# Optimization experiments

Measured on AMD Instinct MI355X. Metric: run time of the kernel, lower is better.

## Reference

```python
import jax, jax.numpy as jnp
import numpy as np

H, NH, R = 128, 8, 6
NB = 2                  # geometric interaction blocks
BS, L, K = 16, 64, 16   # graphs, blocks/graph, atoms/block
NBLK = BS * L           # 1024 blocks total
N = NBLK * K            # 16384 atoms
E = 262144              # atom-level edges
EB = 512                # block-level edges per graph
CUTOFF = 8.0


def _mha(x, in_w, in_b, out_w, out_b):
    # torch nn.MultiheadAttention (batch_first, eval / no dropout). x: [B,S,H]
    B_, S, _ = x.shape
    qkv = x @ in_w + in_b                     # [B,S,3H]
    q, k, v = jnp.split(qkv, 3, axis=-1)
    dh = H // NH
    q = q.reshape(B_, S, NH, dh)
    k = k.reshape(B_, S, NH, dh)
    v = v.reshape(B_, S, NH, dh)
    scores = jnp.einsum('bind,bjnd->bnij', q, k) / np.sqrt(dh).astype(np.float32)
    attn = jax.nn.softmax(scores, axis=-1)
    o = jnp.einsum('bnij,bjnd->bind', attn, v).reshape(B_, S, H)
    return o @ out_w + out_b


def _forward(A, atom_positions, B_types, coords, edge_index, block_edges,
             emb_atom, emb_pos, emb_block, rbf_freq,
             inter_w1, inter_b1, inter_w2, inter_b2,
             upd_w1, upd_b1, upd_w2, upd_b2,
             edge_w1, edge_b1, edge_w2, edge_b2,
             attn_in_w, attn_in_b, attn_out_w, attn_out_b,
             ln_g, ln_b, fin_w1, fin_b1, fin_w2, fin_b2, fin_w3, fin_b3):
    block_id = jnp.repeat(jnp.arange(NBLK), K)  # uniform K atoms per block
    # atom embedding + position embedding + broadcast block embedding
    x = emb_atom[A] + emb_pos[atom_positions] + emb_block[B_types][block_id]  # [N,H]

    # ---- GeometricAtomProcessor ----
    i, j = edge_index[0], edge_index[1]
    d = jnp.linalg.norm(coords[i] - coords[j], axis=-1)       # [E]
    u = jnp.clip(d / CUTOFF, 1e-3, None)
    # DimeNet envelope, exponent=5 -> p=6: 1/u + a u^5 + b u^6 + c u^7
    env = 1.0 / u - 28.0 * u**5 + 48.0 * u**6 - 21.0 * u**7
    rbf = env[:, None] * jnp.sin(rbf_freq[None, :] * u[:, None])  # [E,R]

    for b in range(NB):
        ef = jnp.concatenate([x[i], x[j], rbf], axis=-1)       # [E,2H+R] gather
        m = jax.nn.silu(ef @ inter_w1[b] + inter_b1[b]) @ inter_w2[b] + inter_b2[b]
        agg = jax.ops.segment_sum(m, i, num_segments=N)        # index_add_ scatter
        ui = jnp.concatenate([x, agg], axis=-1)
        x = jax.nn.silu(ui @ upd_w1[b] + upd_b1[b]) @ upd_w2[b] + upd_b2[b] + x

    # scatter_mean over block_id (uniform blocks -> reshape mean)
    blocks = x.reshape(NBLK, K, H).mean(axis=1).reshape(BS, L, H)

    # ---- per-graph block-edge attention (batched over graphs) ----
    src, dst = block_edges[..., 0], block_edges[..., 1]        # [BS,EB]
    bidx = jnp.arange(BS)[:, None]
    ef = jnp.concatenate([blocks[bidx, src], blocks[bidx, dst]], axis=-1)  # [BS,EB,2H]
    ef = jax.nn.relu(ef @ edge_w1 + edge_b1) @ edge_w2 + edge_b2
    ea = _mha(ef, attn_in_w, attn_in_b, attn_out_w, attn_out_b)            # [BS,EB,H]
    seg = (src + bidx * L).reshape(-1)
    sums = jax.ops.segment_sum(ea.reshape(-1, H), seg, num_segments=NBLK)
    cnt = jax.ops.segment_sum(jnp.ones((BS * EB,), ea.dtype), seg, num_segments=NBLK)
    blocks = blocks + (sums / jnp.maximum(cnt, 1.0)[:, None]).reshape(BS, L, H)

    # ---- block self-attention + mean pool ----
    att = _mha(blocks, attn_in_w, attn_in_b, attn_out_w, attn_out_b)
    g = att.mean(axis=1)                                       # [BS,H]
    mu = g.mean(-1, keepdims=True)
    var = ((g - mu) ** 2).mean(-1, keepdims=True)
    g = (g - mu) / jnp.sqrt(var + 1e-5) * ln_g + ln_b
    h1 = jax.nn.relu(g @ fin_w1 + fin_b1)
    h2 = jax.nn.relu(h1 @ fin_w2 + fin_b2)
    return (h2 @ fin_w3 + fin_b3).squeeze(-1)                  # [BS]


def setup_inputs() -> dict:
    key = jax.random.key(0)
    ks = jax.random.split(key, 40)
    def nrm(k, shape, s=0.05):
        return jax.random.normal(k, shape, jnp.float32) * s
    inp = {}
    inp['A'] = jax.random.randint(ks[0], (N,), 0, 100)
    inp['atom_positions'] = jax.random.randint(ks[1], (N,), 0, 16)
    inp['B_types'] = jax.random.randint(ks[2], (NBLK,), 0, 1000)
    inp['coords'] = jax.random.uniform(ks[3], (N, 3), jnp.float32, 0.0, 20.0)
    inp['edge_index'] = jax.random.randint(ks[4], (2, E), 0, N)
    inp['block_edges'] = jax.random.randint(ks[5], (BS, EB, 2), 0, L)
    inp['emb_atom'] = nrm(ks[6], (100, H), 0.5)
    inp['emb_pos'] = nrm(ks[7], (16, H), 0.5)
    inp['emb_block'] = nrm(ks[8], (1000, H), 0.5)
    inp['rbf_freq'] = (jnp.arange(1, R + 1, dtype=jnp.float32) * np.pi)
    inp['inter_w1'] = nrm(ks[9], (NB, 2 * H + R, H))
    inp['inter_b1'] = jnp.zeros((NB, H), jnp.float32)
    inp['inter_w2'] = nrm(ks[10], (NB, H, H))
    inp['inter_b2'] = jnp.zeros((NB, H), jnp.float32)
    inp['upd_w1'] = nrm(ks[11], (NB, 2 * H, H))
    inp['upd_b1'] = jnp.zeros((NB, H), jnp.float32)
    inp['upd_w2'] = nrm(ks[12], (NB, H, H))
    inp['upd_b2'] = jnp.zeros((NB, H), jnp.float32)
    inp['edge_w1'] = nrm(ks[13], (2 * H, H))
    inp['edge_b1'] = jnp.zeros((H,), jnp.float32)
    inp['edge_w2'] = nrm(ks[14], (H, H))
    inp['edge_b2'] = jnp.zeros((H,), jnp.float32)
    inp['attn_in_w'] = nrm(ks[15], (H, 3 * H))
    inp['attn_in_b'] = jnp.zeros((3 * H,), jnp.float32)
    inp['attn_out_w'] = nrm(ks[16], (H, H))
    inp['attn_out_b'] = jnp.zeros((H,), jnp.float32)
    inp['ln_g'] = jnp.ones((H,), jnp.float32)
    inp['ln_b'] = jnp.zeros((H,), jnp.float32)
    inp['fin_w1'] = nrm(ks[17], (H, H))
    inp['fin_b1'] = jnp.zeros((H,), jnp.float32)
    inp['fin_w2'] = nrm(ks[18], (H, H))
    inp['fin_b2'] = jnp.zeros((H,), jnp.float32)
    inp['fin_w3'] = nrm(ks[19], (H, 1))
    inp['fin_b3'] = jnp.zeros((1,), jnp.float32)
    return inp


def reference(A, atom_positions, B_types, coords, edge_index, block_edges,
              emb_atom, emb_pos, emb_block, rbf_freq,
              inter_w1, inter_b1, inter_w2, inter_b2,
              upd_w1, upd_b1, upd_w2, upd_b2,
              edge_w1, edge_b1, edge_w2, edge_b2,
              attn_in_w, attn_in_b, attn_out_w, attn_out_b,
              ln_g, ln_b, fin_w1, fin_b1, fin_w2, fin_b2, fin_w3, fin_b3):
    return _forward(A, atom_positions, B_types, coords, edge_index, block_edges,
                    emb_atom, emb_pos, emb_block, rbf_freq,
                    inter_w1, inter_b1, inter_w2, inter_b2,
                    upd_w1, upd_b1, upd_w2, upd_b2,
                    edge_w1, edge_b1, edge_w2, edge_b2,
                    attn_in_w, attn_in_b, attn_out_w, attn_out_b,
                    ln_g, ln_b, fin_w1, fin_b1, fin_w2, fin_b2, fin_w3, fin_b3)
```

## Files before the change

kernel.cpp:

```cpp
#include <hip/hip_runtime.h>
#include <math.h>

#define H 128
#define NHD 8
#define DH 16
#define RB 6
#define NBI 2
#define BSG 16
#define LBLK 64
#define KATOM 16
#define NBLKT 1024
#define NA 16384
#define NE 262144
#define EBE 512

__device__ __forceinline__ float atomAddF(float* p, float v) {
#if defined(__gfx90a__) || defined(__gfx940__) || defined(__gfx941__) || defined(__gfx942__) || defined(__gfx950__)
  return unsafeAtomicAdd(p, v);
#else
  return atomicAdd(p, v);
#endif
}

__device__ __forceinline__ float fsilu(float v) {
  return v * __builtin_amdgcn_rcpf(1.0f + __expf(-v));
}

typedef short v4s __attribute__((ext_vector_type(4)));
typedef float f32x4 __attribute__((ext_vector_type(4)));

__device__ __forceinline__ short f2bf(float f) {
  union { float f; unsigned u; } v; v.f = f;
  unsigned r = v.u + 0x7fffu + ((v.u >> 16) & 1u);
  return (short)(r >> 16);
}

#if defined(__has_builtin)
#if __has_builtin(__builtin_amdgcn_mfma_f32_16x16x16bf16_1k)
#define HAVE_MFMA16_1K 1
#endif
#endif

#ifdef HAVE_MFMA16_1K
__device__ __forceinline__ f32x4 mfma16(v4s a, v4s b, f32x4 c) {
  return __builtin_amdgcn_mfma_f32_16x16x16bf16_1k(a, b, c, 0, 0, 0);
}
#else
typedef short v8s __attribute__((ext_vector_type(8)));
__device__ __forceinline__ f32x4 mfma16(v4s a, v4s b, f32x4 c) {
  v8s a8 = {a[0], a[1], a[2], a[3], 0, 0, 0, 0};
  v8s b8 = {b[0], b[1], b[2], b[3], 0, 0, 0, 0};
  return __builtin_amdgcn_mfma_f32_16x16x32_bf16(a8, b8, c, 0, 0, 0);
}
#endif

__global__ __launch_bounds__(256) void k_embed(
    const int* __restrict__ A, const int* __restrict__ apos,
    const int* __restrict__ btypes,
    const float* __restrict__ emb_atom, const float* __restrict__ emb_pos,
    const float* __restrict__ emb_block, float* __restrict__ x)
{
  int idx = blockIdx.x * 256 + threadIdx.x;
  int n = idx >> 7, h = idx & 127;
  x[idx] = emb_atom[A[n] * H + h] + emb_pos[apos[n] * H + h]
         + emb_block[btypes[n >> 4] * H + h];
}

__global__ __launch_bounds__(256) void k_hist(
    const int* __restrict__ ei, int* __restrict__ cnt)
{
  int e = blockIdx.x * 256 + threadIdx.x;
  atomicAdd(&cnt[ei[e]], 1);
}

__global__ __launch_bounds__(1024) void k_scan(
    const int* __restrict__ cnt, int* __restrict__ off,
    int* __restrict__ cur, float* __restrict__ cntf)
{
  __shared__ int ps[1024];
  int t = threadIdx.x;
  int base = t * 16;
  int local[16];
  int s = 0;
  #pragma unroll
  for (int k = 0; k < 16; ++k) { local[k] = s; s += cnt[base + k]; }
  ps[t] = s;
  __syncthreads();
  for (int d = 1; d < 1024; d <<= 1) {
    int v = (t >= d) ? ps[t - d] : 0;
    __syncthreads();
    ps[t] += v;
    __syncthreads();
  }
  int offset = (t == 0) ? 0 : ps[t - 1];
  #pragma unroll
  for (int k = 0; k < 16; ++k) {
    int o = offset + local[k];
    off[base + k] = o;
    cur[base + k] = o;
    cntf[base + k] = (float)cnt[base + k];
  }
  if (t == 1023) off[NA] = offset + s;
}

__global__ __launch_bounds__(256) void k_scatter(
    const int* __restrict__ ei, const int* __restrict__ ej,
    const float* __restrict__ coords, const float* __restrict__ freq,
    int* __restrict__ cur, int* __restrict__ ej_s, float* __restrict__ rbf_s)
{
  int e = blockIdx.x * 256 + threadIdx.x;
  int i = ei[e], j = ej[e];
  int pos = atomicAdd(&cur[i], 1);
  ej_s[pos] = j;
  float dx = coords[i*3+0] - coords[j*3+0];
  float dy = coords[i*3+1] - coords[j*3+1];
  float dz = coords[i*3+2] - coords[j*3+2];
  float d = sqrtf(dx*dx + dy*dy + dz*dz);
  float u = fmaxf(d * 0.125f, 1e-3f);
  float u2 = u*u, u4 = u2*u2, u5 = u4*u, u6 = u5*u, u7 = u6*u;
  float env = 1.0f/u - 28.0f*u5 + 48.0f*u6 - 21.0f*u7;
  #pragma unroll
  for (int r = 0; r < RB; ++r)
    rbf_s[(size_t)pos*RB + r] = env * sinf(freq[r] * u);
}

__global__ __launch_bounds__(256) void k_bedge_csr(
    const int* __restrict__ bedges, int* __restrict__ blist,
    int* __restrict__ boff, float* __restrict__ ind)
{
  __shared__ int hist[64], offs[65], curs[64];
  int b = blockIdx.x, t = threadIdx.x;
  if (t < 64) hist[t] = 0;
  __syncthreads();
  for (int e = t; e < EBE; e += 256) atomicAdd(&hist[bedges[(b*EBE + e)*2]], 1);
  __syncthreads();
  if (t == 0) {
    offs[0] = 0;
    for (int k = 0; k < 64; ++k) offs[k+1] = offs[k] + hist[k];
  }
  __syncthreads();
  if (t < 64) curs[t] = offs[t];
  __syncthreads();
  for (int e = t; e < EBE; e += 256) {
    int src = bedges[(b*EBE + e)*2];
    int pos = atomicAdd(&curs[src], 1);
    blist[b*EBE + pos] = e;
  }
  if (t < 65) boff[b*65 + t] = offs[t];
  if (t < 64) ind[b*64 + t] = (hist[t] > 0) ? 1.0f : 0.0f;
}

__global__ __launch_bounds__(256) void k_edge_csr(
    const float* __restrict__ P, const float* __restrict__ Q,
    const float* __restrict__ rbf_s, const float* __restrict__ W1c,
    const int* __restrict__ ej_s, const int* __restrict__ off,
    float* __restrict__ Hagg)
{
  __shared__ float w[RB * H];
  for (int idx = threadIdx.x; idx < RB * H; idx += 256) w[idx] = W1c[idx];
  __syncthreads();
  int c4 = threadIdx.x & 31;
  int sub = threadIdx.x >> 5;
  int i = blockIdx.x * 8 + sub;
  int e0 = off[i], e1 = off[i + 1];
  float4 pv = *(const float4*)&P[(size_t)i * H + c4 * 4];
  float4 W0 = *(const float4*)&w[0*H + c4*4];
  float4 W1 = *(const float4*)&w[1*H + c4*4];
  float4 W2 = *(const float4*)&w[2*H + c4*4];
  float4 W3 = *(const float4*)&w[3*H + c4*4];
  float4 W4 = *(const float4*)&w[4*H + c4*4];
  float4 W5 = *(const float4*)&w[5*H + c4*4];
  float4 acc = {0, 0, 0, 0};
  for (int e = e0; e < e1; ++e) {
    int j = ej_s[e];
    float4 qv = *(const float4*)&Q[(size_t)j * H + c4 * 4];
    const float* rb = &rbf_s[(size_t)e * RB];
    float r0 = rb[0], r1 = rb[1], r2 = rb[2], r3 = rb[3], r4 = rb[4], r5 = rb[5];
    float4 v;
    v.x = pv.x + qv.x + r0*W0.x + r1*W1.x + r2*W2.x + r3*W3.x + r4*W4.x + r5*W5.x;
    v.y = pv.y + qv.y + r0*W0.y + r1*W1.y + r2*W2.y + r3*W3.y + r4*W4.y + r5*W5.y;
    v.z = pv.z + qv.z + r0*W0.z + r1*W1.z + r2*W2.z + r3*W3.z + r4*W4.z + r5*W5.z;
    v.w = pv.w + qv.w + r0*W0.w + r1*W1.w + r2*W2.w + r3*W3.w + r4*W4.w + r5*W5.w;
    acc.x += fsilu(v.x);
    acc.y += fsilu(v.y);
    acc.z += fsilu(v.z);
    acc.w += fsilu(v.w);
  }
  *(float4*)&Hagg[(size_t)i * H + c4 * 4] = acc;
}

__global__ __launch_bounds__(128) void k_wprep(
    const float* __restrict__ W2base, const float* __restrict__ U1base,
    const float* __restrict__ b2base, float* __restrict__ bvecbase,
    short* __restrict__ wt_u1base)
{
  int y = blockIdx.y;
  const float* W2 = W2base + (size_t)y * H * H;
  const float* U1 = U1base + (size_t)y * 2 * H * H;
  const float* b2 = b2base + y * H;
  float* bvec = bvecbase + y * H;
  short* wt1 = wt_u1base + (size_t)y * 128 * 256;
  int k = blockIdx.x, c = threadIdx.x;
  const float* U1b = U1 + 128 * H;
  wt1[c * 256 + k] = f2bf(U1[k * H + c]);
  float s = 0.0f;
  for (int t = 0; t < H; ++t) s += W2[k * H + t] * U1b[t * H + c];
  wt1[c * 256 + 128 + k] = f2bf(s);
  if (k == 0) {
    float sb = 0.0f;
    for (int t = 0; t < H; ++t) sb += b2[t] * U1b[t * H + c];
    bvec[c] = sb;
  }
}

__global__ __launch_bounds__(256) void k_tcvt(
    const float* __restrict__ inter_w1, const float* __restrict__ upd_w2,
    short* __restrict__ wt_pq, short* __restrict__ wt_u2)
{
  int idx = blockIdx.x * 256 + threadIdx.x;
  {
    int k = idx & 127, col = (idx >> 7) & 127, y = (idx >> 14) & 1, b = idx >> 15;
    wt_pq[idx] = f2bf(inter_w1[((size_t)b*262 + y*128 + k)*128 + col]);
  }
  if (idx < 2*128*128) {
    int k = idx & 127, col = (idx >> 7) & 127, b = idx >> 14;
    wt_u2[idx] = f2bf(upd_w2[((size_t)b*128 + k)*128 + col]);
  }
}

__global__ __launch_bounds__(256) void k_pq_mfma(
    const float* __restrict__ x, const short* __restrict__ WtPQ,
    const float* __restrict__ b1,
    float* __restrict__ P, float* __restrict__ Q)
{
  __shared__ short As[64][136];
  __shared__ short Ws[128][72];
  int tid = threadIdx.x;
  int m0 = blockIdx.x * 64;
  int y = blockIdx.y;
  const short* Wt = WtPQ + (size_t)y * 128 * 128;
  float* C = y ? Q : P;
  for (int idx = tid; idx < 64*32; idx += 256) {
    int r = idx >> 5, c4 = idx & 31;
    float4 v = *(const float4*)&x[(size_t)(m0 + r)*H + c4*4];
    short4 s4 = { f2bf(v.x), f2bf(v.y), f2bf(v.z), f2bf(v.w) };
    *(short4*)&As[r][c4*4] = s4;
  }
  int lane = tid & 63, wv = tid >> 6;
  int c = lane & 15, g = lane >> 4;
  int rowb = wv * 16;
  f32x4 acc[8];
  #pragma unroll
  for (int t = 0; t < 8; ++t) acc[t] = (f32x4){0,0,0,0};
  for (int kc = 0; kc < 2; ++kc) {
    __syncthreads();
    {
      int col = tid >> 1, hh = (tid & 1) * 32;
      const int4* src = (const int4*)&Wt[col*128 + kc*64 + hh];
      int4 a0 = src[0], a1 = src[1], a2 = src[2], a3 = src[3];
      *(int4*)&Ws[col][hh] = a0;      *(int4*)&Ws[col][hh+8] = a1;
      *(int4*)&Ws[col][hh+16] = a2;   *(int4*)&Ws[col][hh+24] = a3;
    }
    __syncthreads();
    #pragma unroll
    for (int ks = 0; ks < 4; ++ks) {
      v4s a = *(const v4s*)&As[rowb + c][kc*64 + ks*16 + g*4];
      #pragma unroll
      for (int ct = 0; ct < 8; ++ct) {
        v4s bf = *(const v4s*)&Ws[ct*16 + c][ks*16 + g*4];
        acc[ct] = mfma16(a, bf, acc[ct]);
      }
    }
  }
  #pragma unroll
  for (int ct = 0; ct < 8; ++ct) {
    int col = ct*16 + c;
    float bb = y ? 0.0f : b1[col];
    #pragma unroll
    for (int r = 0; r < 4; ++r) {
      int row = m0 + rowb + g*4 + r;
      C[(size_t)row*H + col] = acc[ct][r] + bb;
    }
  }
}

__global__ __launch_bounds__(256) void k_upd_mfma(
    const float* __restrict__ x, const float* __restrict__ Hagg,
    const short* __restrict__ Wt1,
    const float* __restrict__ b1, const float* __restrict__ bvec,
    const float* __restrict__ cntf,
    const short* __restrict__ Wt2,
    const float* __restrict__ b2,
    float* __restrict__ xout)
{
  __shared__ short As[64][264];
  __shared__ short Ws[128][72];
  __shared__ short Us[64][136];
  int tid = threadIdx.x;
  int m0 = blockIdx.x * 64;
  for (int idx = tid; idx < 64*64; idx += 256) {
    int r = idx >> 6, c4 = idx & 63;
    const float* src = (c4 < 32) ? &x[(size_t)(m0 + r)*H + c4*4]
                                 : &Hagg[(size_t)(m0 + r)*H + (c4-32)*4];
    float4 v = *(const float4*)src;
    short4 s4 = { f2bf(v.x), f2bf(v.y), f2bf(v.z), f2bf(v.w) };
    *(short4*)&As[r][c4*4] = s4;
  }
  int lane = tid & 63, wv = tid >> 6;
  int c = lane & 15, g = lane >> 4;
  int rowb = wv * 16;
  f32x4 acc[8];
  #pragma unroll
  for (int t = 0; t < 8; ++t) acc[t] = (f32x4){0,0,0,0};
  for (int kc = 0; kc < 4; ++kc) {
    __syncthreads();
    {
      int col = tid >> 1, hh = (tid & 1) * 32;
      const int4* src = (const int4*)&Wt1[col*256 + kc*64 + hh];
      int4 a0 = src[0], a1 = src[1], a2 = src[2], a3 = src[3];
      *(int4*)&Ws[col][hh] = a0;      *(int4*)&Ws[col][hh+8] = a1;
      *(int4*)&Ws[col][hh+16] = a2;   *(int4*)&Ws[col][hh+24] = a3;
    }
    __syncthreads();
    #pragma unroll
    for (int ks = 0; ks < 4; ++ks) {
      v4s a = *(const v4s*)&As[rowb + c][kc*64 + ks*16 + g*4];
      #pragma unroll
      for (int ct = 0; ct < 8; ++ct) {
        v4s bf = *(const v4s*)&Ws[ct*16 + c][ks*16 + g*4];
        acc[ct] = mfma16(a, bf, acc[ct]);
      }
    }
  }
  {
    float cr[4];
    #pragma unroll
    for (int r = 0; r < 4; ++r) cr[r] = cntf[m0 + rowb + g*4 + r];
    #pragma unroll
    for (int ct = 0; ct < 8; ++ct) {
      int col = ct*16 + c;
      float bb = b1[col], bv = bvec[col];
      #pragma unroll
      for (int r = 0; r < 4; ++r) {
        float v = acc[ct][r] + bb + bv * cr[r];
        Us[rowb + g*4 + r][col] = f2bf(fsilu(v));
        acc[ct][r] = 0.0f;
      }
    }
  }
  for (int kc = 0; kc < 2; ++kc) {
    __syncthreads();
    {
      int col = tid >> 1, hh = (tid & 1) * 32;
      const int4* src = (const int4*)&Wt2[col*128 + kc*64 + hh];
      int4 a0 = src[0], a1 = src[1], a2 = src[2], a3 = src[3];
      *(int4*)&Ws[col][hh] = a0;      *(int4*)&Ws[col][hh+8] = a1;
      *(int4*)&Ws[col][hh+16] = a2;   *(int4*)&Ws[col][hh+24] = a3;
    }
    __syncthreads();
    #pragma unroll
    for (int ks = 0; ks < 4; ++ks) {
      v4s a = *(const v4s*)&Us[rowb + c][kc*64 + ks*16 + g*4];
      #pragma unroll
      for (int ct = 0; ct < 8; ++ct) {
        v4s bf = *(const v4s*)&Ws[ct*16 + c][ks*16 + g*4];
        acc[ct] = mfma16(a, bf, acc[ct]);
      }
    }
  }
  #pragma unroll
  for (int ct = 0; ct < 8; ++ct) {
    int col = ct*16 + c;
    float bb = b2[col];
    #pragma unroll
    for (int r = 0; r < 4; ++r) {
      int row = m0 + rowb + g*4 + r;
      xout[(size_t)row*H + col] = acc[ct][r] + bb + x[(size_t)row*H + col];
    }
  }
}

__global__ __launch_bounds__(256) void gemm128(
    const float* __restrict__ A1, const float* __restrict__ A2,
    const float* __restrict__ W, int ldw, int wcol0,
    const float* __restrict__ bias, const float* __restrict__ bias2,
    const float* __restrict__ bias_scale,
    const float* __restrict__ res,
    float* __restrict__ C, int ldc, int ccol0,
    int M, int Ktot, int act, int ymul, int wrowmul, long long cymul)
{
  __shared__ float As[32][256];
  __shared__ float Ws[16][128];
  int tid = threadIdx.x;
  int m0 = blockIdx.x * 32;
  int yoff = blockIdx.y * ymul;
  W += (size_t)blockIdx.y * wrowmul * ldw;
  C += (size_t)blockIdx.y * cymul;
  bool doBias = (ymul != 0) || (blockIdx.y == 0);
  for (int idx = tid; idx < 32*32; idx += 256) {
    int r = idx >> 5, k4 = idx & 31;
    float4 v = *(const float4*)&A1[(size_t)(m0 + r)*H + k4*4];
    *(float4*)&As[r][k4*4] = v;
  }
  if (A2) {
    for (int idx = tid; idx < 32*32; idx += 256) {
      int r = idx >> 5, k4 = idx & 31;
      float4 v = *(const float4*)&A2[(size_t)(m0 + r)*H + k4*4];
      *(float4*)&As[r][128 + k4*4] = v;
    }
  }
  int rr = tid >> 5;
  int cq = tid & 31;
  float acc[4][4] = {};
  for (int kk0 = 0; kk0 < Ktot; kk0 += 16) {
    __syncthreads();
    for (int idx = tid; idx < 16*32; idx += 256) {
      int kr = idx >> 5, c4 = idx & 31;
      float4 v = *(const float4*)&W[(size_t)(kk0 + kr)*ldw + wcol0 + yoff + c4*4];
      *(float4*)&Ws[kr][c4*4] = v;
    }
    __syncthreads();
    #pragma unroll
    for (int k4 = 0; k4 < 4; ++k4) {
      float4 w0 = *(const float4*)&Ws[k4*4+0][cq*4];
      float4 w1 = *(const float4*)&Ws[k4*4+1][cq*4];
      float4 w2 = *(const float4*)&Ws[k4*4+2][cq*4];
      float4 w3 = *(const float4*)&Ws[k4*4+3][cq*4];
      #pragma unroll
      for (int i = 0; i < 4; ++i) {
        float4 a = *(const float4*)&As[rr + 8*i][kk0 + k4*4];
        acc[i][0] += a.x*w0.x + a.y*w1.x + a.z*w2.x + a.w*w3.x;
        acc[i][1] += a.x*w0.y + a.y*w1.y + a.z*w2.y + a.w*w3.y;
        acc[i][2] += a.x*w0.z + a.y*w1.z + a.z*w2.z + a.w*w3.z;
        acc[i][3] += a.x*w0.w + a.y*w1.w + a.z*w2.w + a.w*w3.w;
      }
    }
  }
  #pragma unroll
  for (int i = 0; i < 4; ++i) {
    int m = m0 + rr + 8*i;
    float bs = bias_scale ? bias_scale[m] : 1.0f;
    float4 out;
    float* po = &out.x;
    #pragma unroll
    for (int j = 0; j < 4; ++j) {
      int c = cq*4 + j;
      float v = acc[i][j];
      if (bias && doBias) v += bias[yoff + c];
      if (bias2 && doBias) v += bias2[yoff + c] * bs;
      if (act == 1) v = fsilu(v);
      else if (act == 2) v = fmaxf(v, 0.0f);
      if (res) v += res[(size_t)m*H + c];
      po[j] = v;
    }
    *(float4*)&C[(size_t)m*ldc + ccol0 + yoff + cq*4] = out;
  }
}

__global__ __launch_bounds__(256) void k_eprep(
    const float* __restrict__ Pb, const float* __restrict__ Qb,
    const int* __restrict__ bedges,
    const float* __restrict__ W2e, const float* __restrict__ b2e,
    const float* __restrict__ Win, const float* __restrict__ bin,
    float* __restrict__ qkv)
{
  __shared__ float As[32][128];
  __shared__ float Ws[16][128];
  __shared__ float Us[32][128];
  int tid = threadIdx.x;
  int m0 = blockIdx.x * 32;
  int chunk = blockIdx.y;
  for (int idx = tid; idx < 32*32; idx += 256) {
    int r = idx >> 5, k4 = idx & 31;
    int row = m0 + r;
    int g = row >> 9;
    int src = bedges[row*2], dst = bedges[row*2 + 1];
    float4 pv = *(const float4*)&Pb[(size_t)(g*LBLK + src)*H + k4*4];
    float4 qv = *(const float4*)&Qb[(size_t)(g*LBLK + dst)*H + k4*4];
    float4 v;
    v.x = fmaxf(pv.x + qv.x, 0.0f);
    v.y = fmaxf(pv.y + qv.y, 0.0f);
    v.z = fmaxf(pv.z + qv.z, 0.0f);
    v.w = fmaxf(pv.w + qv.w, 0.0f);
    *(float4*)&As[r][k4*4] = v;
  }
  int rr = tid >> 5;
  int cq = tid & 31;
  float acc[4][4] = {};
  for (int kk0 = 0; kk0 < 128; kk0 += 16) {
    __syncthreads();
    for (int idx = tid; idx < 16*32; idx += 256) {
      int kr = idx >> 5, c4 = idx & 31;
      *(float4*)&Ws[kr][c4*4] = *(const float4*)&W2e[(size_t)(kk0 + kr)*H + c4*4];
    }
    __syncthreads();
    #pragma unroll
    for (int k4 = 0; k4 < 4; ++k4) {
      float4 w0 = *(const float4*)&Ws[k4*4+0][cq*4];
      float4 w1 = *(const float4*)&Ws[k4*4+1][cq*4];
      float4 w2 = *(const float4*)&Ws[k4*4+2][cq*4];
      float4 w3 = *(const float4*)&Ws[k4*4+3][cq*4];
      #pragma unroll
      for (int i = 0; i < 4; ++i) {
        float4 a = *(const float4*)&As[rr + 8*i][kk0 + k4*4];
        acc[i][0] += a.x*w0.x + a.y*w1.x + a.z*w2.x + a.w*w3.x;
        acc[i][1] += a.x*w0.y + a.y*w1.y + a.z*w2.y + a.w*w3.y;
        acc[i][2] += a.x*w0.z + a.y*w1.z + a.z*w2.z + a.w*w3.z;
        acc[i][3] += a.x*w0.w + a.y*w1.w + a.z*w2.w + a.w*w3.w;
      }
    }
  }
  #pragma unroll
  for (int i = 0; i < 4; ++i) {
    float4 u;
    float* pu = &u.x;
    #pragma unroll
    for (int j = 0; j < 4; ++j) pu[j] = acc[i][j] + b2e[cq*4 + j];
    *(float4*)&Us[rr + 8*i][cq*4] = u;
    acc[i][0] = 0.0f; acc[i][1] = 0.0f; acc[i][2] = 0.0f; acc[i][3] = 0.0f;
  }
  for (int kk0 = 0; kk0 < 128; kk0 += 16) {
    __syncthreads();
    for (int idx = tid; idx < 16*32; idx += 256) {
      int kr = idx >> 5, c4 = idx & 31;
      *(float4*)&Ws[kr][c4*4] =
          *(const float4*)&Win[(size_t)(kk0 + kr)*384 + chunk*128 + c4*4];
    }
    __syncthreads();
    #pragma unroll
    for (int k4 = 0; k4 < 4; ++k4) {
      float4 w0 = *(const float4*)&Ws[k4*4+0][cq*4];
      float4 w1 = *(const float4*)&Ws[k4*4+1][cq*4];
      float4 w2 = *(const float4*)&Ws[k4*4+2][cq*4];
      float4 w3 = *(const float4*)&Ws[k4*4+3][cq*4];
      #pragma unroll
      for (int i = 0; i < 4; ++i) {
        float4 a = *(const float4*)&Us[rr + 8*i][kk0 + k4*4];
        acc[i][0] += a.x*w0.x + a.y*w1.x + a.z*w2.x + a.w*w3.x;
        acc[i][1] += a.x*w0.y + a.y*w1.y + a.z*w2.y + a.w*w3.y;
        acc[i][2] += a.x*w0.z + a.y*w1.z + a.z*w2.z + a.w*w3.z;
        acc[i][3] += a.x*w0.w + a.y*w1.w + a.z*w2.w + a.w*w3.w;
      }
    }
  }
  #pragma unroll
  for (int i = 0; i < 4; ++i) {
    int m = m0 + rr + 8*i;
    float4 out;
    float* po = &out.x;
    #pragma unroll
    for (int j = 0; j < 4; ++j)
      po[j] = acc[i][j] + bin[chunk*128 + cq*4 + j];
    *(float4*)&qkv[(size_t)m*384 + chunk*128 + cq*4] = out;
  }
}

__global__ __launch_bounds__(256) void k_bprep(
    const float* __restrict__ bsum, const float* __restrict__ Wout,
    const float* __restrict__ bout, const float* __restrict__ ind,
    const float* __restrict__ blocks,
    const float* __restrict__ Win, const float* __restrict__ bin,
    float* __restrict__ qkv)
{
  __shared__ float As[32][128];
  __shared__ float Ws[16][128];
  __shared__ float Us[32][128];
  int tid = threadIdx.x;
  int m0 = blockIdx.x * 32;
  int chunk = blockIdx.y;
  for (int idx = tid; idx < 32*32; idx += 256) {
    int r = idx >> 5, k4 = idx & 31;
    *(float4*)&As[r][k4*4] = *(const float4*)&bsum[(size_t)(m0 + r)*H + k4*4];
  }
  int rr = tid >> 5;
  int cq = tid & 31;
  float acc[4][4] = {};
  for (int kk0 = 0; kk0 < 128; kk0 += 16) {
    __syncthreads();
    for (int idx = tid; idx < 16*32; idx += 256) {
      int kr = idx >> 5, c4 = idx & 31;
      *(float4*)&Ws[kr][c4*4] = *(const float4*)&Wout[(size_t)(kk0 + kr)*H + c4*4];
    }
    __syncthreads();
    #pragma unroll
    for (int k4 = 0; k4 < 4; ++k4) {
      float4 w0 = *(const float4*)&Ws[k4*4+0][cq*4];
      float4 w1 = *(const float4*)&Ws[k4*4+1][cq*4];
      float4 w2 = *(const float4*)&Ws[k4*4+2][cq*4];
      float4 w3 = *(const float4*)&Ws[k4*4+3][cq*4];
      #pragma unroll
      for (int i = 0; i < 4; ++i) {
        float4 a = *(const float4*)&As[rr + 8*i][kk0 + k4*4];
        acc[i][0] += a.x*w0.x + a.y*w1.x + a.z*w2.x + a.w*w3.x;
        acc[i][1] += a.x*w0.y + a.y*w1.y + a.z*w2.y + a.w*w3.y;
        acc[i][2] += a.x*w0.z + a.y*w1.z + a.z*w2.z + a.w*w3.z;
        acc[i][3] += a.x*w0.w + a.y*w1.w + a.z*w2.w + a.w*w3.w;
      }
    }
  }
  #pragma unroll
  for (int i = 0; i < 4; ++i) {
    int m = m0 + rr + 8*i;
    float bs = ind[m];
    float4 u;
    float* pu = &u.x;
    #pragma unroll
    for (int j = 0; j < 4; ++j) {
      int c = cq*4 + j;
      pu[j] = acc[i][j] + bout[c] * bs + blocks[(size_t)m*H + c];
    }
    *(float4*)&Us[rr + 8*i][cq*4] = u;
    acc[i][0] = 0.0f; acc[i][1] = 0.0f; acc[i][2] = 0.0f; acc[i][3] = 0.0f;
  }
  for (int kk0 = 0; kk0 < 128; kk0 += 16) {
    __syncthreads();
    for (int idx = tid; idx < 16*32; idx += 256) {
      int kr = idx >> 5, c4 = idx & 31;
      *(float4*)&Ws[kr][c4*4] =
          *(const float4*)&Win[(size_t)(kk0 + kr)*384 + chunk*128 + c4*4];
    }
    __syncthreads();
    #pragma unroll
    for (int k4 = 0; k4 < 4; ++k4) {
      float4 w0 = *(const float4*)&Ws[k4*4+0][cq*4];
      float4 w1 = *(const float4*)&Ws[k4*4+1][cq*4];
      float4 w2 = *(const float4*)&Ws[k4*4+2][cq*4];
      float4 w3 = *(const float4*)&Ws[k4*4+3][cq*4];
      #pragma unroll
      for (int i = 0; i < 4; ++i) {
        float4 a = *(const float4*)&Us[rr + 8*i][kk0 + k4*4];
        acc[i][0] += a.x*w0.x + a.y*w1.x + a.z*w2.x + a.w*w3.x;
        acc[i][1] += a.x*w0.y + a.y*w1.y + a.z*w2.y + a.w*w3.y;
        acc[i][2] += a.x*w0.z + a.y*w1.z + a.z*w2.z + a.w*w3.z;
        acc[i][3] += a.x*w0.w + a.y*w1.w + a.z*w2.w + a.w*w3.w;
      }
    }
// ... 187 lines not shown
    if (t < off) red[t] += red[t + off];
    __syncthreads();
  }
  float s = red[0];
  __syncthreads();
  return s;
}

__global__ __launch_bounds__(128) void k_final(
    const float* __restrict__ m2, const float* __restrict__ out_w,
    const float* __restrict__ out_b, const float* __restrict__ lng,
    const float* __restrict__ lnb, const float* __restrict__ w1,
    const float* __restrict__ b1, const float* __restrict__ w2,
    const float* __restrict__ b2, const float* __restrict__ w3,
    const float* __restrict__ b3, float* __restrict__ out)
{
  __shared__ float buf[128];
  __shared__ float red[128];
  int b = blockIdx.x, t = threadIdx.x;
  buf[t] = m2[b*H + t];
  __syncthreads();
  float g = out_b[t];
  for (int k = 0; k < H; ++k) g += buf[k] * out_w[k*H + t];
  float mu = bsum128(g, red) * (1.0f / H);
  float df = g - mu;
  float var = bsum128(df * df, red) * (1.0f / H);
  float gn = df / sqrtf(var + 1e-5f) * lng[t] + lnb[t];
  __syncthreads();
  buf[t] = gn; __syncthreads();
  float h1 = b1[t];
  for (int k = 0; k < H; ++k) h1 += buf[k] * w1[k*H + t];
  h1 = fmaxf(h1, 0.0f);
  __syncthreads();
  buf[t] = h1; __syncthreads();
  float h2 = b2[t];
  for (int k = 0; k < H; ++k) h2 += buf[k] * w2[k*H + t];
  h2 = fmaxf(h2, 0.0f);
  float tot = bsum128(h2 * w3[t], red);
  if (t == 0) out[b] = tot + b3[0];
}

extern "C" void kernel_launch(void* const* d_in, const int* in_sizes, int n_in,
                              void* d_out, int out_size, void* d_ws, size_t ws_size,
                              hipStream_t stream) {
  (void)in_sizes; (void)n_in; (void)out_size; (void)ws_size;
  const int*   A          = (const int*)d_in[0];
  const int*   apos       = (const int*)d_in[1];
  const int*   btypes     = (const int*)d_in[2];
  const float* coords     = (const float*)d_in[3];
  const int*   edge_index = (const int*)d_in[4];
  const int*   bedges     = (const int*)d_in[5];
  const float* emb_atom   = (const float*)d_in[6];
  const float* emb_pos    = (const float*)d_in[7];
  const float* emb_block  = (const float*)d_in[8];
  const float* rbf_freq   = (const float*)d_in[9];
  const float* inter_w1   = (const float*)d_in[10];
  const float* inter_b1   = (const float*)d_in[11];
  const float* inter_w2   = (const float*)d_in[12];
  const float* inter_b2   = (const float*)d_in[13];
  const float* upd_w1     = (const float*)d_in[14];
  const float* upd_b1     = (const float*)d_in[15];
  const float* upd_w2     = (const float*)d_in[16];
  const float* upd_b2     = (const float*)d_in[17];
  const float* edge_w1    = (const float*)d_in[18];
  const float* edge_b1    = (const float*)d_in[19];
  const float* edge_w2    = (const float*)d_in[20];
  const float* edge_b2    = (const float*)d_in[21];
  const float* attn_in_w  = (const float*)d_in[22];
  const float* attn_in_b  = (const float*)d_in[23];
  const float* attn_out_w = (const float*)d_in[24];
  const float* attn_out_b = (const float*)d_in[25];
  const float* ln_g       = (const float*)d_in[26];
  const float* ln_b       = (const float*)d_in[27];
  const float* fin_w1     = (const float*)d_in[28];
  const float* fin_b1     = (const float*)d_in[29];
  const float* fin_w2     = (const float*)d_in[30];
  const float* fin_b2     = (const float*)d_in[31];
  const float* fin_w3     = (const float*)d_in[32];
  const float* fin_b3     = (const float*)d_in[33];
  float* out = (float*)d_out;

  float* ws = (float*)d_ws;
  float* x      = ws + 0;
  float* P      = ws + 2097152;
  float* Q      = ws + 4194304;
  float* Hagg   = ws + 6291456;
  float* rbf_s  = ws + 8388608;
  float* cntf   = ws + 9961472;
  float* blocks = ws + 9977856;
  float* Pb     = ws + 10108928;
  float* Qb     = ws + 10240000;
  float* qkv    = ws + 12468224;
  float* bsum   = ws + 15613952;
  float* ind    = ws + 15746048;
  float* m2     = ws + 15747072;
  int* blist    = (int*)(ws + 15749120);
  int* boff     = (int*)(ws + 15757312);
  int* ej_s   = (int*)(ws + 10371072);
  int* off    = (int*)(ws + 10371072 + 262144);
  int* cur    = (int*)(ws + 10371072 + 278784);
  int* cnt    = (int*)(ws + 10371072 + 295168);
  float* bvec = ws + 10371072 + 311552;
  short* wt_pq = (short*)(ws + 12468224);
  short* wt_u1 = (short*)(ws + 12468224 + 32768);
  short* wt_u2 = (short*)(ws + 12468224 + 65536);
  float* ea     = ws + 10371072;

  const int* ei = edge_index;
  const int* ej = edge_index + NE;

  (void)hipMemsetAsync(cnt, 0, NA * sizeof(int), stream);
  k_hist<<<NE/256, 256, 0, stream>>>(ei, cnt);
  k_scan<<<1, 1024, 0, stream>>>(cnt, off, cur, cntf);
  k_scatter<<<NE/256, 256, 0, stream>>>(ei, ej, coords, rbf_freq, cur, ej_s, rbf_s);
  k_bedge_csr<<<BSG, 256, 0, stream>>>(bedges, blist, boff, ind);
  k_wprep<<<dim3(128, 2), 128, 0, stream>>>(inter_w2, upd_w1, inter_b2, bvec, wt_u1);
  k_tcvt<<<256, 256, 0, stream>>>(inter_w1, upd_w2, wt_pq, wt_u2);

  k_embed<<<NA*H/256, 256, 0, stream>>>(A, apos, btypes, emb_atom, emb_pos, emb_block, x);

  for (int b = 0; b < NBI; ++b) {
    const float* w1 = inter_w1 + (size_t)b * 262 * H;
    k_pq_mfma<<<dim3(NA/64, 2), 256, 0, stream>>>(
        x, wt_pq + (size_t)b*2*128*128, inter_b1 + b*H, P, Q);
    k_edge_csr<<<NA/8, 256, 0, stream>>>(P, Q, rbf_s, w1 + 256*H, ej_s, off, Hagg);
    k_upd_mfma<<<NA/64, 256, 0, stream>>>(
        x, Hagg, wt_u1 + (size_t)b*128*256, upd_b1 + b*H, bvec + b*H, cntf,
        wt_u2 + (size_t)b*128*128, upd_b2 + b*H, x);
  }

  k_block_mean<<<NBLKT*H/256, 256, 0, stream>>>(x, blocks);
  gemm128<<<dim3(NBLKT/32, 2), 256, 0, stream>>>(blocks, nullptr, edge_w1, H, 0, edge_b1,
                                                 nullptr, nullptr, nullptr,
                                                 Pb, H, 0, NBLKT, H, 0, 0, 128, 131072);
  k_eprep<<<dim3(BSG*EBE/32, 3), 256, 0, stream>>>(Pb, Qb, bedges, edge_w2, edge_b2,
                                                   attn_in_w, attn_in_b, qkv);
  k_eattn<<<BSG*NHD*(EBE/64), 256, 0, stream>>>(qkv, ea);
  k_bsum_gather<<<NBLKT*32/256, 256, 0, stream>>>(ea, blist, boff, bsum);
  k_bprep<<<dim3(NBLKT/32, 3), 256, 0, stream>>>(bsum, attn_out_w, attn_out_b, ind,
                                                 blocks, attn_in_w, attn_in_b, qkv);
  k_attnS<<<BSG*2, 256, 0, stream>>>(qkv, m2);
  k_final<<<BSG, 128, 0, stream>>>(m2, attn_out_w, attn_out_b, ln_g, ln_b,
                                   fin_w1, fin_b1, fin_w2, fin_b2, fin_w3, fin_b3, out);
}
```

Measured before the change: 430.7 us.

## Store P/Q in bf16 and move block-level edge GEMMs to MFMA

The atom-level P and Q projections are now written as bf16, which halves the gather traffic in the per-edge CSR aggregation kernel, the dominant memory-bound stage. The fp32 SIMT gemm128 and k_eprep for block edges are replaced by bf16 MFMA kernels, with the weights pre-converted in k_tcvt. The transpose-convert setup kernel is reused for this, and sinf is swapped for the fast __sinf intrinsic in the RBF computation. These changes reduce precision in several places, and the weight buffers move to a new workspace offset to avoid overlapping qkv.

```diff
diff --git a/kernel.cpp b/kernel.cpp
--- a/kernel.cpp
+++ b/kernel.cpp
@@ -14,14 +14,6 @@
 #define NE 262144
 #define EBE 512
 
-__device__ __forceinline__ float atomAddF(float* p, float v) {
-#if defined(__gfx90a__) || defined(__gfx940__) || defined(__gfx941__) || defined(__gfx942__) || defined(__gfx950__)
-  return unsafeAtomicAdd(p, v);
-#else
-  return atomicAdd(p, v);
-#endif
-}
-
 __device__ __forceinline__ float fsilu(float v) {
   return v * __builtin_amdgcn_rcpf(1.0f + __expf(-v));
 }
@@ -33,6 +25,12 @@
   union { float f; unsigned u; } v; v.f = f;
   unsigned r = v.u + 0x7fffu + ((v.u >> 16) & 1u);
   return (short)(r >> 16);
+}
+
+__device__ __forceinline__ float bf2f(short s) {
+  union { unsigned u; float f; } v;
+  v.u = ((unsigned)(unsigned short)s) << 16;
+  return v.f;
 }
 
 #if defined(__has_builtin)
@@ -121,7 +119,7 @@
   float env = 1.0f/u - 28.0f*u5 + 48.0f*u6 - 21.0f*u7;
   #pragma unroll
   for (int r = 0; r < RB; ++r)
-    rbf_s[(size_t)pos*RB + r] = env * sinf(freq[r] * u);
+    rbf_s[(size_t)pos*RB + r] = env * __sinf(freq[r] * u);
 }
 
 __global__ __launch_bounds__(256) void k_bedge_csr(
@@ -151,7 +149,7 @@
 }
 
 __global__ __launch_bounds__(256) void k_edge_csr(
-    const float* __restrict__ P, const float* __restrict__ Q,
+    const short* __restrict__ P, const short* __restrict__ Q,
     const float* __restrict__ rbf_s, const float* __restrict__ W1c,
     const int* __restrict__ ej_s, const int* __restrict__ off,
     float* __restrict__ Hagg)
@@ -163,7 +161,8 @@
   int sub = threadIdx.x >> 5;
   int i = blockIdx.x * 8 + sub;
   int e0 = off[i], e1 = off[i + 1];
-  float4 pv = *(const float4*)&P[(size_t)i * H + c4 * 4];
+  short4 p4 = *(const short4*)&P[(size_t)i * H + c4 * 4];
+  float4 pv = { bf2f(p4.x), bf2f(p4.y), bf2f(p4.z), bf2f(p4.w) };
   float4 W0 = *(const float4*)&w[0*H + c4*4];
   float4 W1 = *(const float4*)&w[1*H + c4*4];
   float4 W2 = *(const float4*)&w[2*H + c4*4];
@@ -173,7 +172,8 @@
   float4 acc = {0, 0, 0, 0};
   for (int e = e0; e < e1; ++e) {
     int j = ej_s[e];
-    float4 qv = *(const float4*)&Q[(size_t)j * H + c4 * 4];
+    short4 q4 = *(const short4*)&Q[(size_t)j * H + c4 * 4];
+    float4 qv = { bf2f(q4.x), bf2f(q4.y), bf2f(q4.z), bf2f(q4.w) };
     const float* rb = &rbf_s[(size_t)e * RB];
     float r0 = rb[0], r1 = rb[1], r2 = rb[2], r3 = rb[3], r4 = rb[4], r5 = rb[5];
     float4 v;
@@ -215,7 +215,11 @@
 
 __global__ __launch_bounds__(256) void k_tcvt(
     const float* __restrict__ inter_w1, const float* __restrict__ upd_w2,
-    short* __restrict__ wt_pq, short* __restrict__ wt_u2)
+    const float* __restrict__ edge_w1, const float* __restrict__ edge_w2,
+    const float* __restrict__ attn_in_w,
+    short* __restrict__ wt_pq, short* __restrict__ wt_u2,
+    short* __restrict__ wt_e1, short* __restrict__ wt_e2,
+    short* __restrict__ wt_in)
 {
   int idx = blockIdx.x * 256 + threadIdx.x;
   {
@@ -225,13 +229,22 @@
   if (idx < 2*128*128) {
     int k = idx & 127, col = (idx >> 7) & 127, b = idx >> 14;
     wt_u2[idx] = f2bf(upd_w2[((size_t)b*128 + k)*128 + col]);
+    wt_e1[idx] = f2bf(edge_w1[((size_t)b*128 + k)*128 + col]);
+  }
+  if (idx < 128*128) {
+    int k = idx & 127, col = idx >> 7;
+    wt_e2[idx] = f2bf(edge_w2[(size_t)k*128 + col]);
+  }
+  if (idx < 384*128) {
+    int k = idx & 127, col = idx >> 7;
+    wt_in[idx] = f2bf(attn_in_w[(size_t)k*384 + col]);
   }
 }
 
 __global__ __launch_bounds__(256) void k_pq_mfma(
     const float* __restrict__ x, const short* __restrict__ WtPQ,
     const float* __restrict__ b1,
-    float* __restrict__ P, float* __restrict__ Q)
+    short* __restrict__ P, short* __restrict__ Q)
 {
   __shared__ short As[64][136];
   __shared__ short Ws[128][72];
@@ -239,7 +252,7 @@
   int m0 = blockIdx.x * 64;
   int y = blockIdx.y;
   const short* Wt = WtPQ + (size_t)y * 128 * 128;
-  float* C = y ? Q : P;
+  short* C = y ? Q : P;
   for (int idx = tid; idx < 64*32; idx += 256) {
     int r = idx >> 5, c4 = idx & 31;
     float4 v = *(const float4*)&x[(size_t)(m0 + r)*H + c4*4];
@@ -279,7 +292,7 @@
     #pragma unroll
     for (int r = 0; r < 4; ++r) {
       int row = m0 + rowb + g*4 + r;
-      C[(size_t)row*H + col] = acc[ct][r] + bb;
+      C[(size_t)row*H + col] = f2bf(acc[ct][r] + bb);
     }
   }
 }
@@ -380,178 +393,100 @@
   }
 }
 
-__global__ __launch_bounds__(256) void gemm128(
-    const float* __restrict__ A1, const float* __restrict__ A2,
-    const float* __restrict__ W, int ldw, int wcol0,
-    const float* __restrict__ bias, const float* __restrict__ bias2,
-    const float* __restrict__ bias_scale,
-    const float* __restrict__ res,
-    float* __restrict__ C, int ldc, int ccol0,
-    int M, int Ktot, int act, int ymul, int wrowmul, long long cymul)
-{
-  __shared__ float As[32][256];
-  __shared__ float Ws[16][128];
+__global__ __launch_bounds__(256) void k_eprep_mfma(
+    const short* __restrict__ Pb, const short* __restrict__ Qb,
+    const int* __restrict__ bedges,
+    const short* __restrict__ Wt2e, const float* __restrict__ b2e,
+    const short* __restrict__ WtIn, const float* __restrict__ bin,
+    float* __restrict__ qkv)
+{
+  __shared__ short As[64][136];
+  __shared__ short Ws[128][72];
+  __shared__ short Us[64][136];
   int tid = threadIdx.x;
-  int m0 = blockIdx.x * 32;
-  int yoff = blockIdx.y * ymul;
-  W += (size_t)blockIdx.y * wrowmul * ldw;
-  C += (size_t)blockIdx.y * cymul;
-  bool doBias = (ymul != 0) || (blockIdx.y == 0);
-  for (int idx = tid; idx < 32*32; idx += 256) {
-    int r = idx >> 5, k4 = idx & 31;
-    float4 v = *(const float4*)&A1[(size_t)(m0 + r)*H + k4*4];
-    *(float4*)&As[r][k4*4] = v;
-  }
-  if (A2) {
-    for (int idx = tid; idx < 32*32; idx += 256) {
-      int r = idx >> 5, k4 = idx & 31;
-      float4 v = *(const float4*)&A2[(size_t)(m0 + r)*H + k4*4];
-      *(float4*)&As[r][128 + k4*4] = v;
-    }
-  }
-  int rr = tid >> 5;
-  int cq = tid & 31;
-  float acc[4][4] = {};
-  for (int kk0 = 0; kk0 < Ktot; kk0 += 16) {
-    __syncthreads();
-    for (int idx = tid; idx < 16*32; idx += 256) {
-      int kr = idx >> 5, c4 = idx & 31;
-      float4 v = *(const float4*)&W[(size_t)(kk0 + kr)*ldw + wcol0 + yoff + c4*4];
-      *(float4*)&Ws[kr][c4*4] = v;
-    }
-    __syncthreads();
-    #pragma unroll
-    for (int k4 = 0; k4 < 4; ++k4) {
-      float4 w0 = *(const float4*)&Ws[k4*4+0][cq*4];
-      float4 w1 = *(const float4*)&Ws[k4*4+1][cq*4];
-      float4 w2 = *(const float4*)&Ws[k4*4+2][cq*4];
-      float4 w3 = *(const float4*)&Ws[k4*4+3][cq*4];
-      #pragma unroll
-      for (int i = 0; i < 4; ++i) {
-        float4 a = *(const float4*)&As[rr + 8*i][kk0 + k4*4];
-        acc[i][0] += a.x*w0.x + a.y*w1.x + a.z*w2.x + a.w*w3.x;
-        acc[i][1] += a.x*w0.y + a.y*w1.y + a.z*w2.y + a.w*w3.y;
-        acc[i][2] += a.x*w0.z + a.y*w1.z + a.z*w2.z + a.w*w3.z;
-        acc[i][3] += a.x*w0.w + a.y*w1.w + a.z*w2.w + a.w*w3.w;
-      }
-    }
-  }
-  #pragma unroll
-  for (int i = 0; i < 4; ++i) {
-    int m = m0 + rr + 8*i;
-    float bs = bias_scale ? bias_scale[m] : 1.0f;
-    float4 out;
-    float* po = &out.x;
-    #pragma unroll
-    for (int j = 0; j < 4; ++j) {
-      int c = cq*4 + j;
-      float v = acc[i][j];
-      if (bias && doBias) v += bias[yoff + c];
-      if (bias2 && doBias) v += bias2[yoff + c] * bs;
-      if (act == 1) v = fsilu(v);
-      else if (act == 2) v = fmaxf(v, 0.0f);
-      if (res) v += res[(size_t)m*H + c];
-      po[j] = v;
-    }
-    *(float4*)&C[(size_t)m*ldc + ccol0 + yoff + cq*4] = out;
-  }
-}
-
-__global__ __launch_bounds__(256) void k_eprep(
-    const float* __restrict__ Pb, const float* __restrict__ Qb,
-    const int* __restrict__ bedges,
-    const float* __restrict__ W2e, const float* __restrict__ b2e,
-    const float* __restrict__ Win, const float* __restrict__ bin,
-    float* __restrict__ qkv)
-{
-  __shared__ float As[32][128];
-  __shared__ float Ws[16][128];
-  __shared__ float Us[32][128];
-  int tid = threadIdx.x;
-  int m0 = blockIdx.x * 32;
-  int chunk = blockIdx.y;
-  for (int idx = tid; idx < 32*32; idx += 256) {
-    int r = idx >> 5, k4 = idx & 31;
+  int m0 = blockIdx.x * 64;
+  for (int idx = tid; idx < 64*32; idx += 256) {
+    int r = idx >> 5, c4 = idx & 31;
     int row = m0 + r;
     int g = row >> 9;
     int src = bedges[row*2], dst = bedges[row*2 + 1];
-    float4 pv = *(const float4*)&Pb[(size_t)(g*LBLK + src)*H + k4*4];
-    float4 qv = *(const float4*)&Qb[(size_t)(g*LBLK + dst)*H + k4*4];
-    float4 v;
-    v.x = fmaxf(pv.x + qv.x, 0.0f);
-    v.y = fmaxf(pv.y + qv.y, 0.0f);
-    v.z = fmaxf(pv.z + qv.z, 0.0f);
-    v.w = fmaxf(pv.w + qv.w, 0.0f);
-    *(float4*)&As[r][k4*4] = v;
-  }
-  int rr = tid >> 5;
-  int cq = tid & 31;
-  float acc[4][4] = {};
-  for (int kk0 = 0; kk0 < 128; kk0 += 16) {
-    __syncthreads();
-    for (int idx = tid; idx < 16*32; idx += 256) {
-      int kr = idx >> 5, c4 = idx & 31;
-      *(float4*)&Ws[kr][c4*4] = *(const float4*)&W2e[(size_t)(kk0 + kr)*H + c4*4];
-    }
-    __syncthreads();
-    #pragma unroll
-    for (int k4 = 0; k4 < 4; ++k4) {
-      float4 w0 = *(const float4*)&Ws[k4*4+0][cq*4];
-      float4 w1 = *(const float4*)&Ws[k4*4+1][cq*4];
-      float4 w2 = *(const float4*)&Ws[k4*4+2][cq*4];
-      float4 w3 = *(const float4*)&Ws[k4*4+3][cq*4];
+    short4 p4 = *(const short4*)&Pb[(size_t)(g*LBLK + src)*H + c4*4];
+    short4 q4 = *(const short4*)&Qb[(size_t)(g*LBLK + dst)*H + c4*4];
+    short4 s4;
+    s4.x = f2bf(fmaxf(bf2f(p4.x) + bf2f(q4.x), 0.0f));
+    s4.y = f2bf(fmaxf(bf2f(p4.y) + bf2f(q4.y), 0.0f));
+    s4.z = f2bf(fmaxf(bf2f(p4.z) + bf2f(q4.z), 0.0f));
+    s4.w = f2bf(fmaxf(bf2f(p4.w) + bf2f(q4.w), 0.0f));
+    *(short4*)&As[r][c4*4] = s4;
+  }
+  int lane = tid & 63, wv = tid >> 6;
+  int c = lane & 15, g = lane >> 4;
+  int rowb = wv * 16;
+  f32x4 acc[8];
+  #pragma unroll
+  for (int t = 0; t < 8; ++t) acc[t] = (f32x4){0,0,0,0};
+  for (int kc = 0; kc < 2; ++kc) {
+    __syncthreads();
+    {
+      int col = tid >> 1, hh = (tid & 1) * 32;
+      const int4* src = (const int4*)&Wt2e[col*128 + kc*64 + hh];
+      int4 a0 = src[0], a1 = src[1], a2 = src[2], a3 = src[3];
+      *(int4*)&Ws[col][hh] = a0;      *(int4*)&Ws[col][hh+8] = a1;
+      *(int4*)&Ws[col][hh+16] = a2;   *(int4*)&Ws[col][hh+24] = a3;
+    }
+    __syncthreads();
+    #pragma unroll
+    for (int ks = 0; ks < 4; ++ks) {
+      v4s a = *(const v4s*)&As[rowb + c][kc*64 + ks*16 + g*4];
       #pragma unroll
-      for (int i = 0; i < 4; ++i) {
-        float4 a = *(const float4*)&As[rr + 8*i][kk0 + k4*4];
-        acc[i][0] += a.x*w0.x + a.y*w1.x + a.z*w2.x + a.w*w3.x;
-        acc[i][1] += a.x*w0.y + a.y*w1.y + a.z*w2.y + a.w*w3.y;
-        acc[i][2] += a.x*w0.z + a.y*w1.z + a.z*w2.z + a.w*w3.z;
-        acc[i][3] += a.x*w0.w + a.y*w1.w + a.z*w2.w + a.w*w3.w;
+      for (int ct = 0; ct < 8; ++ct) {
+        v4s bf = *(const v4s*)&Ws[ct*16 + c][ks*16 + g*4];
+        acc[ct] = mfma16(a, bf, acc[ct]);
       }
     }
   }
   #pragma unroll
-  for (int i = 0; i < 4; ++i) {
-    float4 u;
-    float* pu = &u.x;
-    #pragma unroll
-    for (int j = 0; j < 4; ++j) pu[j] = acc[i][j] + b2e[cq*4 + j];
-    *(float4*)&Us[rr + 8*i][cq*4] = u;
-    acc[i][0] = 0.0f; acc[i][1] = 0.0f; acc[i][2] = 0.0f; acc[i][3] = 0.0f;
-  }
-  for (int kk0 = 0; kk0 < 128; kk0 += 16) {
-    __syncthreads();
-    for (int idx = tid; idx < 16*32; idx += 256) {
-      int kr = idx >> 5, c4 = idx & 31;
-      *(float4*)&Ws[kr][c4*4] =
-          *(const float4*)&Win[(size_t)(kk0 + kr)*384 + chunk*128 + c4*4];
-    }
-    __syncthreads();
-    #pragma unroll
-    for (int k4 = 0; k4 < 4; ++k4) {
-      float4 w0 = *(const float4*)&Ws[k4*4+0][cq*4];
-      float4 w1 = *(const float4*)&Ws[k4*4+1][cq*4];
-      float4 w2 = *(const float4*)&Ws[k4*4+2][cq*4];
-      float4 w3 = *(const float4*)&Ws[k4*4+3][cq*4];
+  for (int ct = 0; ct < 8; ++ct) {
+    int col = ct*16 + c;
+    float bb = b2e[col];
+    #pragma unroll
+    for (int r = 0; r < 4; ++r) {
+      Us[rowb + g*4 + r][col] = f2bf(acc[ct][r] + bb);
+      acc[ct][r] = 0.0f;
+    }
+  }
+  for (int cc = 0; cc < 3; ++cc) {
+    for (int kc = 0; kc < 2; ++kc) {
+      __syncthreads();
+      {
+        int col = tid >> 1, hh = (tid & 1) * 32;
+        const int4* src = (const int4*)&WtIn[(size_t)(cc*128 + col)*128 + kc*64 + hh];
+        int4 a0 = src[0], a1 = src[1], a2 = src[2], a3 = src[3];
+        *(int4*)&Ws[col][hh] = a0;      *(int4*)&Ws[col][hh+8] = a1;
+        *(int4*)&Ws[col][hh+16] = a2;   *(int4*)&Ws[col][hh+24] = a3;
+      }
+      __syncthreads();
       #pragma unroll
-      for (int i = 0; i < 4; ++i) {
-        float4 a = *(const float4*)&Us[rr + 8*i][kk0 + k4*4];
-        acc[i][0] += a.x*w0.x + a.y*w1.x + a.z*w2.x + a.w*w3.x;
-        acc[i][1] += a.x*w0.y + a.y*w1.y + a.z*w2.y + a.w*w3.y;
-        acc[i][2] += a.x*w0.z + a.y*w1.z + a.z*w2.z + a.w*w3.z;
-        acc[i][3] += a.x*w0.w + a.y*w1.w + a.z*w2.w + a.w*w3.w;
+      for (int ks = 0; ks < 4; ++ks) {
+        v4s a = *(const v4s*)&Us[rowb + c][kc*64 + ks*16 + g*4];
+        #pragma unroll
+        for (int ct = 0; ct < 8; ++ct) {
+          v4s bf = *(const v4s*)&Ws[ct*16 + c][ks*16 + g*4];
+          acc[ct] = mfma16(a, bf, acc[ct]);
+        }
       }
     }
-  }
-  #pragma unroll
-  for (int i = 0; i < 4; ++i) {
-    int m = m0 + rr + 8*i;
-    float4 out;
-    float* po = &out.x;
-    #pragma unroll
-    for (int j = 0; j < 4; ++j)
-      po[j] = acc[i][j] + bin[chunk*128 + cq*4 + j];
-    *(float4*)&qkv[(size_t)m*384 + chunk*128 + cq*4] = out;
+    #pragma unroll
+    for (int ct = 0; ct < 8; ++ct) {
+      int col = ct*16 + c;
+      float bb = bin[cc*128 + col];
+      #pragma unroll
+      for (int r = 0; r < 4; ++r) {
+        int row = m0 + rowb + g*4 + r;
+        qkv[(size_t)row*384 + cc*128 + col] = acc[ct][r] + bb;
+        acc[ct][r] = 0.0f;
+      }
+    }
   }
 }
 
@@ -905,14 +840,14 @@
 
   float* ws = (float*)d_ws;
   float* x      = ws + 0;
-  float* P      = ws + 2097152;
-  float* Q      = ws + 4194304;
+  short* P      = (short*)(ws + 2097152);
+  short* Q      = (short*)(ws + 4194304);
   float* Hagg   = ws + 6291456;
   float* rbf_s  = ws + 8388608;
   float* cntf   = ws + 9961472;
   float* blocks = ws + 9977856;
-  float* Pb     = ws + 10108928;
-  float* Qb     = ws + 10240000;
+  short* Pb     = (short*)(ws + 10108928);
+  short* Qb     = (short*)(ws + 10240000);
   float* qkv    = ws + 12468224;
   float* bsum   = ws + 15613952;
   float* ind    = ws + 15746048;
@@ -924,9 +859,12 @@
   int* cur    = (int*)(ws + 10371072 + 278784);
   int* cnt    = (int*)(ws + 10371072 + 295168);
   float* bvec = ws + 10371072 + 311552;
-  short* wt_pq = (short*)(ws + 12468224);
-  short* wt_u1 = (short*)(ws + 12468224 + 32768);
-  short* wt_u2 = (short*)(ws + 12468224 + 65536);
+  short* wt_pq = (short*)(ws + 16777216);
+  short* wt_u1 = (short*)(ws + 16777216 + 32768);
+  short* wt_u2 = (short*)(ws + 16777216 + 65536);
+  short* wt_e1 = (short*)(ws + 16777216 + 81920);
+  short* wt_e2 = (short*)(ws + 16777216 + 98304);
+  short* wt_in = (short*)(ws + 16777216 + 106496);
   float* ea     = ws + 10371072;
 
   const int* ei = edge_index;
@@ -938,7 +876,8 @@
   k_scatter<<<NE/256, 256, 0, stream>>>(ei, ej, coords, rbf_freq, cur, ej_s, rbf_s);
   k_bedge_csr<<<BSG, 256, 0, stream>>>(bedges, blist, boff, ind);
   k_wprep<<<dim3(128, 2), 128, 0, stream>>>(inter_w2, upd_w1, inter_b2, bvec, wt_u1);
-  k_tcvt<<<256, 256, 0, stream>>>(inter_w1, upd_w2, wt_pq, wt_u2);
+  k_tcvt<<<256, 256, 0, stream>>>(inter_w1, upd_w2, edge_w1, edge_w2, attn_in_w,
+                                  wt_pq, wt_u2, wt_e1, wt_e2, wt_in);
 
   k_embed<<<NA*H/256, 256, 0, stream>>>(A, apos, btypes, emb_atom, emb_pos, emb_block, x);
 
@@ -953,11 +892,9 @@
   }
 
   k_block_mean<<<NBLKT*H/256, 256, 0, stream>>>(x, blocks);
-  gemm128<<<dim3(NBLKT/32, 2), 256, 0, stream>>>(blocks, nullptr, edge_w1, H, 0, edge_b1,
-                                                 nullptr, nullptr, nullptr,
-                                                 Pb, H, 0, NBLKT, H, 0, 0, 128, 131072);
-  k_eprep<<<dim3(BSG*EBE/32, 3), 256, 0, stream>>>(Pb, Qb, bedges, edge_w2, edge_b2,
-                                                   attn_in_w, attn_in_b, qkv);
+  k_pq_mfma<<<dim3(NBLKT/64, 2), 256, 0, stream>>>(blocks, wt_e1, edge_b1, Pb, Qb);
+  k_eprep_mfma<<<BSG*EBE/64, 256, 0, stream>>>(Pb, Qb, bedges, wt_e2, edge_b2,
+                                               wt_in, attn_in_b, qkv);
   k_eattn<<<BSG*NHD*(EBE/64), 256, 0, stream>>>(qkv, ea);
   k_bsum_gather<<<NBLKT*32/256, 256, 0, stream>>>(ea, blist, boff, bsum);
   k_bprep<<<dim3(NBLKT/32, 3), 256, 0, stream>>>(bsum, attn_out_w, attn_out_b, ind,
```

After: 398.8 us. 1.08x faster.
